# Performance work log

Hardware: AMD Instinct MI355X
Metric: run time of the kernel (lower is better)

The kernel has to match this reference:

```python
import jax, jax.numpy as jnp
import numpy as np

EPS = 2.220446049250313e-16  # sys.float_info.epsilon, matches CoCosNet feature_normalize

def feature_normalize(x):
    return x / (jnp.linalg.norm(x, axis=1, keepdims=True) + EPS)

def conv1x1(x, w, b):  # w: (out, in)
    return jnp.einsum('bchw,oc->bohw', x, w) + b[None, :, None, None]

def conv3x3(x, w, b):  # w: (out, in, 3, 3), SAME padding, stride 1
    y = jax.lax.conv_general_dilated(x, w, (1, 1), 'SAME',
                                     dimension_numbers=('NCHW', 'OIHW', 'NCHW'))
    return y + b[None, :, None, None]

@jax.custom_vjp
def sign_sig(x):
    return (x > 0).astype(x.dtype)

def _ss_fwd(x):
    return (x > 0).astype(x.dtype), jax.nn.sigmoid(x)

def _ss_bwd(s, g):
    return (g * s * (1.0 - s),)

sign_sig.defvjp(_ss_fwd, _ss_bwd)

def pono(x, eps=1e-5):  # PositionalNorm2d: normalize over channel dim
    m = jnp.mean(x, axis=1, keepdims=True)
    v = jnp.var(x, axis=1, keepdims=True)
    return (x - m) * jax.lax.rsqrt(v + eps)

def instance_norm(x, eps=1e-5):  # param-free, over spatial dims
    m = jnp.mean(x, axis=(2, 3), keepdims=True)
    v = jnp.var(x, axis=(2, 3), keepdims=True)
    return (x - m) * jax.lax.rsqrt(v + eps)

def setup_inputs() -> dict:
    B, CV, CPOS, H, W = 2, 256, 64, 64, 64
    CQK, DP, IC, NH = CV + CPOS, 64, 3, 128
    key = jax.random.key(0)
    ks = jax.random.split(key, 24)
    n = lambda i, s: jax.random.normal(ks[i], s, jnp.float32)
    w = lambda i, s: n(i, s) * 0.02
    z = lambda s: jnp.zeros(s, jnp.float32)
    return dict(
        q=n(0, (B, CV, H, W)), k=n(1, (B, CV, H, W)), v=n(2, (B, CV, H, W)),
        pos=n(3, (1, CPOS, H, W)),
        seg_map=jax.random.uniform(ks[4], (B, IC, H, W), jnp.float32),
        v2=n(5, (B, CV, H, W)),
        f_w=w(6, (CQK, CQK)), f_b=z(CQK),
        g_w=w(7, (CQK, CQK)), g_b=z(CQK),
        h_w=w(8, (CV, CV)), h_b=z(CV),
        fp_w=w(9, (DP, CQK)), fp_b=z(DP),
        gp_w=w(10, (DP, CQK)), gp_b=z(DP),
        sp_s_w=w(11, (NH, IC, 3, 3)), sp_s_b=z(NH),
        sp_g_w=w(12, (CV, NH, 3, 3)), sp_g_b=z(CV),
        sp_b_w=w(13, (CV, NH, 3, 3)), sp_b_b=z(CV),
        r1_w=w(14, (CV, CV, 3, 3)), r1_b=z(CV),
        r2_w=w(15, (CV, CV, 3, 3)), r2_b=z(CV),
    )

def reference(q, k, v, pos, seg_map, v2,
              f_w, f_b, g_w, g_b, h_w, h_b, fp_w, fp_b, gp_w, gp_b,
              sp_s_w, sp_s_b, sp_g_w, sp_g_b, sp_b_w, sp_b_b,
              r1_w, r1_b, r2_w, r2_b):
    b, cv, h, w = q.shape
    posb = jnp.broadcast_to(pos, (b,) + pos.shape[1:])
    query = jnp.concatenate([feature_normalize(q), posb], axis=1)
    keyt = jnp.concatenate([feature_normalize(k), posb], axis=1)
    qf = conv1x1(query, f_w, f_b)
    kf = conv1x1(keyt, g_w, g_b)
    vh = conv1x1(v, h_w, h_b)
    qp = conv1x1(query, fp_w, fp_b)
    kp = conv1x1(keyt, gp_w, gp_b)
    cqk = qf.shape[1]
    n = h * w
    Q = qf.reshape(b, cqk, n).transpose(0, 2, 1)          # (b, N, c_qk)
    K = kf.reshape(b, cqk, n)                             # (b, c_qk, N)
    V = vh.reshape(b, cv, n).transpose(0, 2, 1)           # (b, N, c_v)
    Qp = qp.reshape(b, -1, n).transpose(0, 2, 1)
    Kp = kp.reshape(b, -1, n)
    mask = sign_sig(jnp.einsum('bnc,bcm->bnm', Qp, Kp) / Kp.shape[1])
    cor = jnp.einsum('bnc,bcm->bnm', Q, K) / jnp.sqrt(jnp.float32(cqk))
    attn = jax.nn.softmax(cor, axis=-1)
    masked = attn * mask
    out = jnp.einsum('bnm,bmc->bnc', masked, V).transpose(0, 2, 1).reshape(b, cv, h, w)
    conf = masked.sum(-1).reshape(b, 1, h, w)
    V2 = v2.reshape(b, -1, n).transpose(0, 2, 1)
    attn2 = jax.nn.softmax(jnp.where(mask > 0, jnp.float32(-10000.0), cor), axis=-1)
    out2 = jnp.einsum('bnm,bmc->bnc', attn2, V2).transpose(0, 2, 1).reshape(b, -1, h, w)
    # SPADE(q, seg_map)
    actv = jax.nn.relu(conv3x3(seg_map, sp_s_w, sp_s_b))
    spade = instance_norm(q) * (1.0 + conv3x3(actv, sp_g_w, sp_g_b)) + conv3x3(actv, sp_b_w, sp_b_b)
    y = pono(out + (1.0 - conf) * spade + q)
    res = y + conv3x3(jax.nn.relu(conv3x3(y, r1_w, r1_b)), r2_w, r2_b)
    return (res, out2, cor)
```

## Files before the change

### kernel.cpp

```cpp
#include <hip/hip_runtime.h>
#include <stdint.h>


#define DEV static __device__ __forceinline__

typedef short short8 __attribute__((ext_vector_type(8)));
typedef float floatx4 __attribute__((ext_vector_type(4)));

DEV float bf2f(unsigned short b) { return __uint_as_float(((unsigned int)b) << 16); }
DEV unsigned short f2bf(float f) {
  unsigned int u = __float_as_uint(f);
  u += 0x7FFFu + ((u >> 16) & 1u);
  return (unsigned short)(u >> 16);
}
DEV float bfround(float f) { return bf2f(f2bf(f)); }

__global__ __launch_bounds__(256)
void cvt_f2b(const float* __restrict__ in, unsigned short* __restrict__ out, int n)
{
  int i = blockIdx.x * 256 + threadIdx.x;
  if (i < n) out[i] = f2bf(in[i]);
}

__global__ __launch_bounds__(256)
void prep_w9(const float* __restrict__ w, unsigned short* __restrict__ w9,
             int CO, int CI)
{
  int i = blockIdx.x * 256 + threadIdx.x;
  int tot = CO * CI * 9;
  if (i >= tot) return;
  int s = i % 9, rest = i / 9;
  int ci = rest % CI, o = rest / CI;
  w9[(long long)o * 9 * CI + s * CI + ci] = f2bf(w[i]);
}

__global__ __launch_bounds__(256)
void colnorm(const float* __restrict__ x, float* __restrict__ rnorm)
{
  int b = blockIdx.y, t = threadIdx.x;
  int n = (blockIdx.x << 5) + (t & 31);
  int cg = t >> 5;
  const float* base = x + ((long long)b << 20) + n;
  float s = 0.f;
#pragma unroll
  for (int c8 = 0; c8 < 32; c8++) {
    float v = base[((long long)(cg * 32 + c8)) << 12];
    s += v * v;
  }
  __shared__ float red[256];
  red[t] = s; __syncthreads();
  for (int st = 128; st >= 32; st >>= 1) {
    if (t < st) red[t] += red[t + st];
    __syncthreads();
  }
  if (t < 32)
    rnorm[(b << 12) + n] = 1.f / (sqrtf(red[t]) + 2.2204460492503131e-16f);
}

__global__ __launch_bounds__(256)
void build_qk3(const float* __restrict__ x, const float* __restrict__ pos,
               const float* __restrict__ rnorm, unsigned short* __restrict__ qt)
{
  __shared__ float tile[64][65];
  int b = blockIdx.z, by = blockIdx.y;
  int n0 = blockIdx.x << 6;
  int tx = threadIdx.x & 63, tg = threadIdx.x >> 6;
  const float* ib;
  int c0;
  if (by < 4) { ib = x + ((long long)b << 20) + ((long long)(by << 6) << 12); c0 = by << 6; }
  else        { ib = pos; c0 = 256; }
#pragma unroll
  for (int i = 0; i < 16; i++) {
    int r = tg * 16 + i;
    tile[r][tx] = ib[((long long)r << 12) + n0 + tx];
  }
  __syncthreads();
#pragma unroll
  for (int i = 0; i < 16; i++) {
    int r = tg * 16 + i;
    float sc = (by < 4) ? rnorm[(b << 12) + n0 + r] : 1.f;
    qt[((long long)(b * 4096 + n0 + r)) * 320 + c0 + tx] = f2bf(tile[tx][r] * sc);
  }
}

__global__ __launch_bounds__(256)
void transpose_c(const float* __restrict__ in, unsigned short* __restrict__ out, int C)
{
  __shared__ float tile[64][65];
  int b = blockIdx.z;
  int c0 = blockIdx.y << 6;
  int n0 = blockIdx.x << 6;
  const float* ib = in + (long long)b * C * 4096;
  unsigned short* ob = out + (long long)b * C * 4096;
  int tx = threadIdx.x & 63, tg = threadIdx.x >> 6;
#pragma unroll
  for (int i = 0; i < 16; i++) {
    int r = tg * 16 + i;
    tile[r][tx] = ib[((long long)(c0 + r) << 12) + n0 + tx];
  }
  __syncthreads();
#pragma unroll
  for (int i = 0; i < 16; i++) {
    int r = tg * 16 + i;
    ob[(long long)(n0 + r) * C + c0 + tx] = f2bf(tile[tx][r]);
  }
}

__global__ __launch_bounds__(256)
void gemm_bt(const unsigned short* __restrict__ A, long long sAb, int lda,
             const unsigned short* __restrict__ Bt, long long sBb, int ldb,
             int Ncols, int K, float alpha,
             const float* __restrict__ bias, int biasMode,
             unsigned short* __restrict__ Cb, long long sCbb, int ldcb,
             float* __restrict__ Cf, long long sCfb, int ldcf,
             unsigned short* __restrict__ Cm)
{
  __shared__ unsigned short As[128][40];
  __shared__ unsigned short Bs[128][40];
  int bz = blockIdx.z;
  const unsigned short* Ab = A + bz * sAb;
  const unsigned short* Bb = Bt + bz * sBb;
  int m0 = blockIdx.y << 7, n0 = blockIdx.x << 7;
  int t = threadIdx.x;
  int lane = t & 63, wave = t >> 6, quad = lane >> 4, l16 = lane & 15;
  int wm = (wave >> 1) << 6, wn = (wave & 1) << 6;

  floatx4 acc[4][4] = {};

  for (int k0 = 0; k0 < K; k0 += 32) {
#pragma unroll
    for (int s = 0; s < 2; s++) {
      int idx = t + (s << 8);
      int row = idx >> 2, ch = (idx & 3) << 3;
      short8 av = *(const short8*)(Ab + (long long)(m0 + row) * lda + k0 + ch);
      *(short8*)&As[row][ch] = av;
      short8 bv = {};
      if (n0 + row < Ncols) bv = *(const short8*)(Bb + (long long)(n0 + row) * ldb + k0 + ch);
      *(short8*)&Bs[row][ch] = bv;
    }
    __syncthreads();
    short8 af[4], bfv[4];
#pragma unroll
    for (int i = 0; i < 4; i++) af[i] = *(const short8*)&As[wm + (i << 4) + l16][quad << 3];
#pragma unroll
    for (int j = 0; j < 4; j++) bfv[j] = *(const short8*)&Bs[wn + (j << 4) + l16][quad << 3];
#pragma unroll
    for (int i = 0; i < 4; i++)
#pragma unroll
      for (int j = 0; j < 4; j++)
        acc[i][j] = __builtin_amdgcn_mfma_f32_16x16x32_bf16(af[i], bfv[j], acc[i][j], 0, 0, 0);
    __syncthreads();
  }

#pragma unroll
  for (int j = 0; j < 4; j++) {
    int col = n0 + wn + (j << 4) + l16;
    if (col >= Ncols) continue;
    float bcol = (biasMode == 1) ? bias[col] : 0.f;
#pragma unroll
    for (int i = 0; i < 4; i++) {
#pragma unroll
      for (int r = 0; r < 4; r++) {
        int row = m0 + wm + (i << 4) + (quad << 2) + r;
        float vv = acc[i][j][r] * alpha + bcol;
        if (biasMode == 2) vv += bias[row];
        if (Cb) Cb[bz * sCbb + (long long)row * ldcb + col] = f2bf(vv);
        if (Cf) Cf[bz * sCfb + (long long)row * ldcf + col] = bfround(vv);
        if (Cm) {
          unsigned long long bal = __ballot(vv > 0.f);
          if (l16 == 0)
            Cm[(long long)bz * 4096 * 256 + (long long)row * 256 + ((n0 + wn + (j << 4)) >> 4)]
              = (unsigned short)(bal >> (quad << 4));
        }
      }
    }
  }
}

__global__ __launch_bounds__(256)
void gemm_conv(const unsigned short* __restrict__ Xt, int CI,
               const unsigned short* __restrict__ W9, int CO,
               const float* __restrict__ bias,
               unsigned short* __restrict__ Cb, int relu,
               float* __restrict__ Cf, const float* __restrict__ addT, int rnd)
{
  __shared__ unsigned short As[128][40];
  __shared__ unsigned short Bs[128][40];
  int bz = blockIdx.z;
  const unsigned short* Xb = Xt + (long long)bz * 4096 * CI;
  int m0 = blockIdx.y << 7, n0 = blockIdx.x << 7;
  int t = threadIdx.x;
  int lane = t & 63, wave = t >> 6, quad = lane >> 4, l16 = lane & 15;
  int wm = (wave >> 1) << 6, wn = (wave & 1) << 6;
  int K9 = 9 * CI;

  floatx4 acc[4][4] = {};

  for (int tap = 0; tap < 9; ++tap) {
    int dy = tap / 3 - 1, dx = tap % 3 - 1;
    int off = dy * 64 + dx;
    for (int kc = 0; kc < CI; kc += 32) {
#pragma unroll
      for (int s = 0; s < 2; s++) {
        int idx = t + (s << 8);
        int row = idx >> 2, ch = (idx & 3) << 3;
        int p = m0 + row;
        int y = (p >> 6) + dy, x = (p & 63) + dx;
        short8 av = {};
        if ((unsigned)y < 64u && (unsigned)x < 64u)
          av = *(const short8*)(Xb + (long long)(p + off) * CI + kc + ch);
        *(short8*)&As[row][ch] = av;
        short8 bv = *(const short8*)(W9 + (long long)(n0 + row) * K9 + tap * CI + kc + ch);
        *(short8*)&Bs[row][ch] = bv;
      }
      __syncthreads();
      short8 af[4], bfv[4];
#pragma unroll
      for (int i = 0; i < 4; i++) af[i] = *(const short8*)&As[wm + (i << 4) + l16][quad << 3];
#pragma unroll
      for (int j = 0; j < 4; j++) bfv[j] = *(const short8*)&Bs[wn + (j << 4) + l16][quad << 3];
#pragma unroll
      for (int i = 0; i < 4; i++)
#pragma unroll
        for (int j = 0; j < 4; j++)
          acc[i][j] = __builtin_amdgcn_mfma_f32_16x16x32_bf16(af[i], bfv[j], acc[i][j], 0, 0, 0);
      __syncthreads();
    }
  }

#pragma unroll
  for (int j = 0; j < 4; j++) {
    int col = n0 + wn + (j << 4) + l16;
    float bcol = bias[col];
#pragma unroll
    for (int i = 0; i < 4; i++) {
#pragma unroll
      for (int r = 0; r < 4; r++) {
        int row = m0 + wm + (i << 4) + (quad << 2) + r;
        float vv = acc[i][j][r] + bcol;
        if (relu) vv = fmaxf(vv, 0.f);
        if (Cb) Cb[((long long)bz * 4096 + row) * CO + col] = f2bf(vv);
        if (Cf) {
          long long oi = ((long long)bz * CO + col) * 4096 + row;
          float ov = vv;
          if (addT) ov += addT[oi];
          Cf[oi] = rnd ? bfround(ov) : ov;
        }
      }
    }
  }
}

__global__ __launch_bounds__(256)
void stats_rows(const float* __restrict__ corF,
                const unsigned char* __restrict__ mbits,
                float4* __restrict__ statA, float* __restrict__ confF)
{
  long long row = blockIdx.x;
  const float4* cr = (const float4*)(corF + (row << 12));
  const unsigned char* mr = mbits + row * 512;
  int t = threadIdx.x;

  float lg[16]; unsigned int mk[16];
#pragma unroll
  for (int i = 0; i < 4; i++) {
    float4 cc = cr[i * 256 + t];
    unsigned char mb = mr[(i * 256 + t) >> 1];
    int sh = (t & 1) << 2;
    lg[4 * i + 0] = cc.x; lg[4 * i + 1] = cc.y;
    lg[4 * i + 2] = cc.z; lg[4 * i + 3] = cc.w;
#pragma unroll
    for (int j = 0; j < 4; j++) mk[4 * i + j] = (mb >> (sh + j)) & 1u;
  }
  float m1 = -3.0e38f, m2 = -3.0e38f; int cnt = 0;
#pragma unroll
  for (int e = 0; e < 16; e++) {
    m1 = fmaxf(m1, lg[e]);
    if (!mk[e]) m2 = fmaxf(m2, lg[e]);
    cnt += (int)mk[e];
  }
  __shared__ float4 red4[256];
  red4[t] = make_float4(m1, m2, 0.f, 0.f); __syncthreads();
  for (int s = 128; s > 0; s >>= 1) {
    if (t < s) {
      red4[t].x = fmaxf(red4[t].x, red4[t + s].x);
      red4[t].y = fmaxf(red4[t].y, red4[t + s].y);
    }
    __syncthreads();
  }
  float rmax1 = red4[0].x;
  float rmax2 = fmaxf(red4[0].y, -10000.f);
  __syncthreads();

  float s1 = 0.f, cn = 0.f, s2 = 0.f;
#pragma unroll
  for (int e = 0; e < 16; e++) {
    float ex = __expf(fminf(lg[e] - rmax1, 0.f));
    s1 += ex;
    if (mk[e]) cn += ex;
    else s2 += __expf(fminf(lg[e] - rmax2, 0.f));
  }
  red4[t] = make_float4(s1, cn, s2, (float)cnt); __syncthreads();
  for (int s = 128; s > 0; s >>= 1) {
    if (t < s) {
      red4[t].x += red4[t + s].x; red4[t].y += red4[t + s].y;
      red4[t].z += red4[t + s].z; red4[t].w += red4[t + s].w;
    }
    __syncthreads();
  }
  if (t == 0) {
    float4 r = red4[0];
    float sum2 = r.z + r.w * __expf(fminf(-10000.f - rmax2, 0.f));
    statA[row] = make_float4(rmax1, 1.f / fmaxf(r.x, 1e-30f),
                             rmax2, 1.f / fmaxf(sum2, 1e-30f));
    confF[row] = r.y / fmaxf(r.x, 1e-30f);
  }
}

__global__ __launch_bounds__(128, 3)
void gemm_pv3(const float* __restrict__ corF,
              const unsigned char* __restrict__ mbits,
              const float4* __restrict__ statA,
              const unsigned short* __restrict__ Bt0,
              const unsigned short* __restrict__ Bt1,
              float* __restrict__ Cf0, float* __restrict__ Cf1)
{
  __shared__ unsigned short As[32][40];
  __shared__ unsigned short Bs[128][40];
  int bz = blockIdx.z & 1, mode = blockIdx.z >> 1;
  const float* corb = corF + (long long)bz * 4096 * 4096;
  const unsigned char* mbb = mbits + (long long)bz * 4096 * 512;
  const unsigned short* Bb = (mode ? Bt1 : Bt0) + (long long)bz * 256 * 4096;
  int m0 = blockIdx.y << 5, n0 = blockIdx.x << 7;
  int t = threadIdx.x;
  int lane = t & 63, wave = t >> 6, quad = lane >> 4, l16 = lane & 15;
  int wn = wave << 6;

  int rA = t >> 2, cA = (t & 3) << 3;

  float4 sS = statA[(long long)bz * 4096 + m0 + rA];
  float rm, iv, mv;
  if (mode == 0) { rm = sS.x; iv = sS.y; mv = 0.f; }
  else { rm = sS.z; iv = sS.w; mv = __expf(fminf(-10000.f - rm, 0.f)) * iv; }

  floatx4 acc[2][4] = {};

  const float* cp_base = corb + (long long)(m0 + rA) * 4096 + cA;
  const unsigned char* mb_base = mbb + (long long)(m0 + rA) * 512 + (cA >> 3);
  const unsigned short* pb_base = Bb + (long long)(n0 + rA) * 4096 + cA;

  float4 pa0, pa1; short8 pb[4]; unsigned char pmb;
  auto issue = [&](int kk) {
    pa0 = *(const float4*)(cp_base + kk);
    pa1 = *(const float4*)(cp_base + kk + 4);
    pmb = mb_base[kk >> 3];
#pragma unroll
    for (int j = 0; j < 4; j++)
      pb[j] = *(const short8*)(pb_base + (long long)(j << 5) * 4096 + kk);
  };

  issue(0);
  for (int k0 = 0; k0 < 4096; k0 += 32) {
    {
      float cs[8] = {pa0.x, pa0.y, pa0.z, pa0.w, pa1.x, pa1.y, pa1.z, pa1.w};
      short8 av;
#pragma unroll
      for (int j = 0; j < 8; j++) {
        float p = __expf(cs[j] - rm) * iv;
        unsigned int mkb = (pmb >> j) & 1u;
        float val = mode ? (mkb ? mv : p) : (mkb ? p : 0.f);
        av[j] = (short)f2bf(val);
      }
      *(short8*)&As[rA][cA] = av;
#pragma unroll
      for (int j = 0; j < 4; j++)
        *(short8*)&Bs[rA + (j << 5)][cA] = pb[j];
    }
    __syncthreads();
    if (k0 + 32 < 4096) issue(k0 + 32);
    short8 af[2], bfv[4];
#pragma unroll
    for (int i = 0; i < 2; i++) af[i] = *(const short8*)&As[(i << 4) + l16][quad << 3];
#pragma unroll
    for (int j = 0; j < 4; j++) bfv[j] = *(const short8*)&Bs[wn + (j << 4) + l16][quad << 3];
#pragma unroll
    for (int i = 0; i < 2; i++)
#pragma unroll
      for (int j = 0; j < 4; j++)
        acc[i][j] = __builtin_amdgcn_mfma_f32_16x16x32_bf16(af[i], bfv[j], acc[i][j], 0, 0, 0);
    __syncthreads();
  }

#pragma unroll
  for (int j = 0; j < 4; j++) {
    int col = n0 + wn + (j << 4) + l16;
#pragma unroll
    for (int i = 0; i < 2; i++) {
#pragma unroll
      for (int r = 0; r < 4; r++) {
        int row = m0 + (i << 4) + (quad << 2) + r;
        float vv = bfround(acc[i][j][r]);
        if (mode) Cf1[(long long)bz * 256 * 4096 + (long long)col * 4096 + row] = vv;
        else      Cf0[(long long)bz * 4096 * 256 + (long long)row * 256 + col] = vv;
      }
    }
  }
}

__global__ __launch_bounds__(256)
void inorm_stats(const float* __restrict__ q, float* __restrict__ mu, float* __restrict__ rs)
{
  int c = blockIdx.x, b = blockIdx.y, t = threadIdx.x;
  const float* base = q + ((long long)(b * 256 + c) << 12);
  float s = 0.f, s2 = 0.f;
  for (int i = t; i < 4096; i += 256) { float v = base[i]; s += v; s2 += v * v; }
  __shared__ float r1[256], r2[256];
  r1[t] = s; r2[t] = s2; __syncthreads();
  for (int st = 128; st > 0; st >>= 1) {
    if (t < st) { r1[t] += r1[t + st]; r2[t] += r2[t + st]; }
    __syncthreads();
  }
  if (t == 0) {
    float m = r1[0] * (1.f / 4096.f);
    float var = fmaxf(r2[0] * (1.f / 4096.f) - m * m, 0.f);
    mu[b * 256 + c] = m;
    rs[b * 256 + c] = rsqrtf(var + 1e-5f);
  }
}

__global__ __launch_bounds__(256)
void conv3x3(const float* __restrict__ inF,
             const float* __restrict__ wgt, const float* __restrict__ bias,
             int CI, int CO, const float* __restrict__ addF,
             float* __restrict__ outF, int relu, int rnd)
{
  __shared__ float wsm[2304];
  int b = blockIdx.z, o = blockIdx.y, t = threadIdx.x;
  for (int i = t; i < CI * 9; i += 256) wsm[i] = wgt[(long long)o * CI * 9 + i];
  __syncthreads();
  int x = t & 63, y = (blockIdx.x << 2) + (t >> 6);
  bool ym = y > 0, yp = y < 63, xm = x > 0, xp = x < 63;
  int p = y * 64 + x;
  long long ibase = ((long long)b * CI) << 12;
  float acc = bias[o];
  for (int ci = 0; ci < CI; ci++) {
    const float* wp = &wsm[ci * 9];
    long long ib = ibase + ((long long)ci << 12) + p;
    float v00 = (ym && xm) ? inF[ib - 65] : 0.f;
    float v01 = ym ? inF[ib - 64] : 0.f;
    float v02 = (ym && xp) ? inF[ib - 63] : 0.f;
    float v10 = xm ? inF[ib - 1] : 0.f;
    float v11 = inF[ib];
    float v12 = xp ? inF[ib + 1] : 0.f;
    float v20 = (yp && xm) ? inF[ib + 63] : 0.f;
    float v21 = yp ? inF[ib + 64] : 0.f;
    float v22 = (yp && xp) ? inF[ib + 65] : 0.f;
    acc += v00 * wp[0] + v01 * wp[1] + v02 * wp[2]
         + v10 * wp[3] + v11 * wp[4] + v12 * wp[5]
         + v20 * wp[6] + v21 * wp[7] + v22 * wp[8];
  }
  if (relu) acc = fmaxf(acc, 0.f);
  long long oidx = (((long long)(b * CO + o)) << 12) + p;
  if (addF) acc += addF[oidx];
  outF[oidx] = rnd ? bfround(acc) : acc;
}

__global__ __launch_bounds__(256)
void pono_y(const float* __restrict__ outF, const float* __restrict__ confF,
            const float* __restrict__ gF, const float* __restrict__ bF,
            const float* __restrict__ q, const float* __restrict__ mu,
            const float* __restrict__ rs, float* __restrict__ yF,
            unsigned short* __restrict__ yT)
{
  int n = blockIdx.x, b = blockIdx.y, c = threadIdx.x;
  long long cn = ((long long)(b * 256 + c) << 12) + n;
  float qv = q[cn];
  float sp = (qv - mu[b * 256 + c]) * rs[b * 256 + c] * (1.f + gF[cn]) + bF[cn];
  float cf = confF[b * 4096 + n];
  float tv = outF[((long long)(b * 4096 + n) << 8) + c] + (1.f - cf) * sp + qv;
  __shared__ float red[256];
  red[c] = tv; __syncthreads();
  for (int s = 128; s > 0; s >>= 1) { if (c < s) red[c] += red[c + s]; __syncthreads(); }
  float m = red[0] * (1.f / 256.f); __syncthreads();
  float d = tv - m;
  red[c] = d * d; __syncthreads();
  for (int s = 128; s > 0; s >>= 1) { if (c < s) red[c] += red[c + s]; __syncthreads(); }
  float var = fmaxf(red[0] * (1.f / 256.f), 0.f);
  float yv = d * rsqrtf(var + 1e-5f);
  yF[cn] = yv;
  yT[((long long)(b * 4096 + n) << 8) + c] = f2bf(yv);
}


extern "C" void kernel_launch(void* const* d_in, const int* in_sizes, int n_in,
                              void* d_out, int out_size, void* d_ws, size_t ws_size,
                              hipStream_t stream)
{
  (void)in_sizes; (void)n_in; (void)out_size; (void)ws_size;
  const int B = 2, CV = 256, CQK = 320, DP = 64, N = 4096, NH = 128, IC = 3;
  const float INV_SQRT_CQK = 0.05590169943749474241f;

  const float* q    = (const float*)d_in[0];
  const float* k    = (const float*)d_in[1];
  const float* v    = (const float*)d_in[2];
  const float* pos  = (const float*)d_in[3];
  const float* seg  = (const float*)d_in[4];
  const float* v2   = (const float*)d_in[5];
  const float* f_w  = (const float*)d_in[6];
  const float* f_b  = (const float*)d_in[7];
  const float* g_w  = (const float*)d_in[8];
  const float* g_b  = (const float*)d_in[9];
  const float* h_w  = (const float*)d_in[10];
  const float* h_b  = (const float*)d_in[11];
  const float* fp_w = (const float*)d_in[12];
  const float* fp_b = (const float*)d_in[13];
  const float* gp_w = (const float*)d_in[14];
  const float* gp_b = (const float*)d_in[15];
  const float* sp_s_w = (const float*)d_in[16];
  const float* sp_s_b = (const float*)d_in[17];
  const float* sp_g_w = (const float*)d_in[18];
  const float* sp_g_b = (const float*)d_in[19];
  const float* sp_b_w = (const float*)d_in[20];
  const float* sp_b_b = (const float*)d_in[21];
  const float* r1_w = (const float*)d_in[22];
  const float* r1_b = (const float*)d_in[23];
  const float* r2_w = (const float*)d_in[24];
  const float* r2_b = (const float*)d_in[25];

  float* res_o  = (float*)d_out;
  float* out2_o = res_o + (long long)B * CV * N;
  float* cor_o  = res_o + 2ll * B * CV * N;

  unsigned short* query_t = (unsigned short*)cor_o;
  unsigned short* keyt_t  = query_t + (long long)B * N * CQK;
  float*          outBuf  = res_o;

  char* wp_ = (char*)d_ws;
  auto take = [&](size_t bytes) -> void* {
    void* r = wp_; wp_ += (bytes + 255) & ~(size_t)255; return r;
  };
  unsigned short* v_t     = (unsigned short*)take((size_t)B * N * CV * 2);
  unsigned short* qf_t    = (unsigned short*)take((size_t)B * N * CQK * 2);
  unsigned short* kf_t    = (unsigned short*)take((size_t)B * N * CQK * 2);
  unsigned short* qp_t    = (unsigned short*)take((size_t)B * N * DP * 2);
  unsigned short* kp_t    = (unsigned short*)take((size_t)B * N * DP * 2);
  unsigned short* vh      = (unsigned short*)take((size_t)B * CV * N * 2);
  unsigned short* v2b     = (unsigned short*)take((size_t)B * CV * N * 2);
  unsigned short* fwB     = (unsigned short*)take((size_t)CQK * CQK * 2);
  unsigned short* gwB     = (unsigned short*)take((size_t)CQK * CQK * 2);
  unsigned short* fpwB    = (unsigned short*)take((size_t)DP * CQK * 2);
  unsigned short* gpwB    = (unsigned short*)take((size_t)DP * CQK * 2);
  unsigned short* hwB     = (unsigned short*)take((size_t)CV * CV * 2);
  unsigned short* maskB16 = (unsigned short*)take((size_t)B * N * 256 * 2);
  float4*         statA   = (float4*)take((size_t)B * N * 16);
  float*          confF   = (float*)take((size_t)B * N * 4);
  float*          muF     = (float*)take((size_t)B * CV * 4);
  float*          rsF     = (float*)take((size_t)B * CV * 4);
  float*          rnormQ  = (float*)take((size_t)B * N * 4);
  float*          rnormK  = (float*)take((size_t)B * N * 4);
  float*          actv    = (float*)take((size_t)B * NH * N * 4);
  float*          gC      = (float*)take((size_t)B * CV * N * 4);
  float*          bC      = (float*)take((size_t)B * CV * N * 4);
  float*          yF      = (float*)take((size_t)B * CV * N * 4);
  unsigned short* spgW9   = (unsigned short*)take((size_t)CV * 9 * NH * 2);
  unsigned short* spbW9   = (unsigned short*)take((size_t)CV * 9 * NH * 2);
  unsigned short* r1W9    = (unsigned short*)take((size_t)CV * 9 * CV * 2);
  unsigned short* r2W9    = (unsigned short*)take((size_t)CV * 9 * CV * 2);
  unsigned short* yT      = qf_t;
  unsigned short* a1T     = kf_t;
  unsigned short* actvT   = v_t;

  dim3 blk(256);
  auto cvt = [&](const float* in, unsigned short* out, int n) {
    cvt_f2b<<<dim3((n + 255) / 256), blk, 0, stream>>>(in, out, n);
  };
  auto prepw = [&](const float* w, unsigned short* w9, int CO, int CI) {
    prep_w9<<<dim3((CO * CI * 9 + 255) / 256), blk, 0, stream>>>(w, w9, CO, CI);
  };
  auto gemm = [&](const unsigned short* A, long long sAb, int lda,
                  const unsigned short* Bt, long long sBb, int ldb,
                  int M, int Nc, int K, float alpha,
                  const float* bias, int biasMode,
                  unsigned short* Cb, long long sCbb, int ldcb,
                  float* Cf, long long sCfb, int ldcf,
                  unsigned short* Cm) {
    dim3 grid((Nc + 127) / 128, M / 128, B);
    gemm_bt<<<grid, blk, 0, stream>>>(A, sAb, lda, Bt, sBb, ldb, Nc, K, alpha,
                                      bias, biasMode, Cb, sCbb, ldcb,
                                      Cf, sCfb, ldcf, Cm);
  };
  auto conv = [&](const unsigned short* Xt, int CI, const unsigned short* W9,
                  const float* bias, unsigned short* Cb, int relu,
                  float* Cf, const float* addT, int rnd) {
    gemm_conv<<<dim3(CV / 128, N / 128, B), blk, 0, stream>>>(
        Xt, CI, W9, CV, bias, Cb, relu, Cf, addT, rnd);
  };

  cvt(f_w, fwB, CQK * CQK);
  cvt(g_w, gwB, CQK * CQK);
  cvt(fp_w, fpwB, DP * CQK);
  cvt(gp_w, gpwB, DP * CQK);
  cvt(h_w, hwB, CV * CV);
  cvt(v2, v2b, B * CV * N);
  prepw(sp_g_w, spgW9, CV, NH);
  prepw(sp_b_w, spbW9, CV, NH);
  prepw(r1_w, r1W9, CV, CV);
  prepw(r2_w, r2W9, CV, CV);

  colnorm<<<dim3(128, B), blk, 0, stream>>>(q, rnormQ);
  colnorm<<<dim3(128, B), blk, 0, stream>>>(k, rnormK);
  build_qk3<<<dim3(64, 5, B), blk, 0, stream>>>(q, pos, rnormQ, query_t);
  build_qk3<<<dim3(64, 5, B), blk, 0, stream>>>(k, pos, rnormK, keyt_t);
  transpose_c<<<dim3(64, 4, B), blk, 0, stream>>>(v, v_t, CV);

  gemm(query_t, (long long)N * CQK, CQK, fwB, 0, CQK, N, CQK, CQK, 1.f, f_b, 1,
       qf_t, (long long)N * CQK, CQK, nullptr, 0, 0, nullptr);
  gemm(keyt_t, (long long)N * CQK, CQK, gwB, 0, CQK, N, CQK, CQK, 1.f, g_b, 1,
       kf_t, (long long)N * CQK, CQK, nullptr, 0, 0, nullptr);
  gemm(query_t, (long long)N * CQK, CQK, fpwB, 0, CQK, N, DP, CQK, 1.f, fp_b, 1,
       qp_t, (long long)N * DP, DP, nullptr, 0, 0, nullptr);
  gemm(keyt_t, (long long)N * CQK, CQK, gpwB, 0, CQK, N, DP, CQK, 1.f, gp_b, 1,
       kp_t, (long long)N * DP, DP, nullptr, 0, 0, nullptr);
  gemm(hwB, 0, CV, v_t, (long long)N * CV, CV, CV, N, CV, 1.f, h_b, 2,
       vh, (long long)CV * N, N, nullptr, 0, 0, nullptr);

  gemm(qf_t, (long long)N * CQK, CQK, kf_t, (long long)N * CQK, CQK, N, N, CQK,
       INV_SQRT_CQK, nullptr, 0, nullptr, 0, 0,
       cor_o, (long long)N * N, N, nullptr);
  gemm(qp_t, (long long)N * DP, DP, kp_t, (long long)N * DP, DP, N, N, DP, 1.f,
       nullptr, 0, nullptr, 0, 0, nullptr, 0, 0, maskB16);

  stats_rows<<<dim3(B * N), blk, 0, stream>>>(cor_o, (const unsigned char*)maskB16,
                                              statA, confF);
  gemm_pv3<<<dim3(2, 128, 2 * B), dim3(128), 0, stream>>>(
      cor_o, (const unsigned char*)maskB16, statA, vh, v2b, outBuf, out2_o);

  inorm_stats<<<dim3(CV, B), blk, 0, stream>>>(q, muF, rsF);
  conv3x3<<<dim3(16, NH, B), blk, 0, stream>>>(seg, sp_s_w, sp_s_b, IC, NH, nullptr, actv, 1, 0);
  transpose_c<<<dim3(64, 2, B), blk, 0, stream>>>(actv, actvT, NH);
  conv(actvT, NH, spgW9, sp_g_b, nullptr, 0, gC, nullptr, 0);
  conv(actvT, NH, spbW9, sp_b_b, nullptr, 0, bC, nullptr, 0);
  pono_y<<<dim3(N, B), blk, 0, stream>>>(outBuf, confF, gC, bC, q, muF, rsF, yF, yT);
  conv(yT, CV, r1W9, r1_b, a1T, 1, nullptr, nullptr, 0);
  conv(a1T, CV, r2W9, r2_b, nullptr, 0, res_o, yF, 1);
}
```

Before: 838.7 us.

## Widen PV GEMM tile to full 256 columns and defer softmax normalization

The fused softmax-times-V kernel now uses 256-thread blocks that cover all 256 output columns per 32-row tile. Each exp(cor) tile is therefore computed once, where before it was recomputed for each of two column halves. The 1/sum normalization moves from the per-element exp to the epilogue, and the exponent uses exp2f with a prescaled log2e. Conversion to bf16 uses the packed v_cvt_pk_bf16_f32 instruction. The block count halves and the LDS B tile doubles, which may lower occupancy. Applying the normalization after accumulation in bf16 slightly changes rounding.

```diff
diff --git a/kernel.cpp b/kernel.cpp
--- a/kernel.cpp
+++ b/kernel.cpp
@@ -317,8 +317,8 @@
   }
 }
 
-__global__ __launch_bounds__(128, 3)
-void gemm_pv3(const float* __restrict__ corF,
+__global__ __launch_bounds__(256, 2)
+void gemm_pv4(const float* __restrict__ corF,
               const unsigned char* __restrict__ mbits,
               const float4* __restrict__ statA,
               const unsigned short* __restrict__ Bt0,
@@ -326,55 +326,64 @@
               float* __restrict__ Cf0, float* __restrict__ Cf1)
 {
   __shared__ unsigned short As[32][40];
-  __shared__ unsigned short Bs[128][40];
-  int bz = blockIdx.z & 1, mode = blockIdx.z >> 1;
+  __shared__ unsigned short Bs[256][40];
+  __shared__ float2 sstat[32];
+  int bz = blockIdx.y & 1, mode = blockIdx.y >> 1;
   const float* corb = corF + (long long)bz * 4096 * 4096;
   const unsigned char* mbb = mbits + (long long)bz * 4096 * 512;
   const unsigned short* Bb = (mode ? Bt1 : Bt0) + (long long)bz * 256 * 4096;
-  int m0 = blockIdx.y << 5, n0 = blockIdx.x << 7;
+  int m0 = blockIdx.x << 5;
   int t = threadIdx.x;
   int lane = t & 63, wave = t >> 6, quad = lane >> 4, l16 = lane & 15;
   int wn = wave << 6;
-
-  int rA = t >> 2, cA = (t & 3) << 3;
-
-  float4 sS = statA[(long long)bz * 4096 + m0 + rA];
-  float rm, iv, mv;
-  if (mode == 0) { rm = sS.x; iv = sS.y; mv = 0.f; }
-  else { rm = sS.z; iv = sS.w; mv = __expf(fminf(-10000.f - rm, 0.f)) * iv; }
+  const float L2E = 1.44269504088896340736f;
+
+  if (t < 32) {
+    float4 s = statA[(long long)bz * 4096 + m0 + t];
+    float rm = mode ? s.z : s.x, iv = mode ? s.w : s.y;
+    sstat[t] = make_float2(-rm * L2E, iv);
+  }
+  __syncthreads();
+
+  int rA = t >> 3, cA = (t & 7) << 2;
+  int rB = t >> 2, cB = (t & 3) << 3;
+  float nrmL = sstat[rA].x;
+  float mvr = exp2f(-10000.f * L2E + nrmL);
 
   floatx4 acc[2][4] = {};
 
-  const float* cp_base = corb + (long long)(m0 + rA) * 4096 + cA;
-  const unsigned char* mb_base = mbb + (long long)(m0 + rA) * 512 + (cA >> 3);
-  const unsigned short* pb_base = Bb + (long long)(n0 + rA) * 4096 + cA;
-
-  float4 pa0, pa1; short8 pb[4]; unsigned char pmb;
+  const float* cpb = corb + (long long)(m0 + rA) * 4096 + cA;
+  const unsigned char* mbp = mbb + (long long)(m0 + rA) * 512;
+  const unsigned short* pbb = Bb + (long long)rB * 4096 + cB;
+
+  float4 pa; short8 pb[4]; unsigned int pmk;
   auto issue = [&](int kk) {
-    pa0 = *(const float4*)(cp_base + kk);
-    pa1 = *(const float4*)(cp_base + kk + 4);
-    pmb = mb_base[kk >> 3];
+    pa = *(const float4*)(cpb + kk);
+    pmk = (unsigned int)(mbp[(kk + cA) >> 3] >> (cA & 7)) & 0xFu;
 #pragma unroll
     for (int j = 0; j < 4; j++)
-      pb[j] = *(const short8*)(pb_base + (long long)(j << 5) * 4096 + kk);
+      pb[j] = *(const short8*)(pbb + (long long)(j << 6) * 4096 + kk);
   };
 
   issue(0);
   for (int k0 = 0; k0 < 4096; k0 += 32) {
     {
-      float cs[8] = {pa0.x, pa0.y, pa0.z, pa0.w, pa1.x, pa1.y, pa1.z, pa1.w};
-      short8 av;
-#pragma unroll
-      for (int j = 0; j < 8; j++) {
-        float p = __expf(cs[j] - rm) * iv;
-        unsigned int mkb = (pmb >> j) & 1u;
-        float val = mode ? (mkb ? mv : p) : (mkb ? p : 0.f);
-        av[j] = (short)f2bf(val);
+      float cs[4] = {pa.x, pa.y, pa.z, pa.w};
+      float vs[4];
+#pragma unroll
+      for (int j = 0; j < 4; j++) {
+        float e = exp2f(fmaf(cs[j], L2E, nrmL));
+        bool mk = (pmk >> j) & 1u;
+        vs[j] = mode ? (mk ? mvr : e) : (mk ? e : 0.f);
       }
-      *(short8*)&As[rA][cA] = av;
+      unsigned int u01, u23;
+      asm("v_cvt_pk_bf16_f32 %0, %1, %2" : "=v"(u01) : "v"(vs[0]), "v"(vs[1]));
+      asm("v_cvt_pk_bf16_f32 %0, %1, %2" : "=v"(u23) : "v"(vs[2]), "v"(vs[3]));
+      *(unsigned int*)&As[rA][cA] = u01;
+      *(unsigned int*)&As[rA][cA + 2] = u23;
 #pragma unroll
       for (int j = 0; j < 4; j++)
-        *(short8*)&Bs[rA + (j << 5)][cA] = pb[j];
+        *(short8*)&Bs[rB + (j << 6)][cB] = pb[j];
     }
     __syncthreads();
     if (k0 + 32 < 4096) issue(k0 + 32);
@@ -393,13 +402,14 @@
 
 #pragma unroll
   for (int j = 0; j < 4; j++) {
-    int col = n0 + wn + (j << 4) + l16;
+    int col = wn + (j << 4) + l16;
 #pragma unroll
     for (int i = 0; i < 2; i++) {
 #pragma unroll
       for (int r = 0; r < 4; r++) {
-        int row = m0 + (i << 4) + (quad << 2) + r;
-        float vv = bfround(acc[i][j][r]);
+        int lrow = (i << 4) + (quad << 2) + r;
+        int row = m0 + lrow;
+        float vv = bfround(acc[i][j][r] * sstat[lrow].y);
         if (mode) Cf1[(long long)bz * 256 * 4096 + (long long)col * 4096 + row] = vv;
         else      Cf0[(long long)bz * 4096 * 256 + (long long)row * 256 + col] = vv;
       }
@@ -632,7 +642,7 @@
 
   stats_rows<<<dim3(B * N), blk, 0, stream>>>(cor_o, (const unsigned char*)maskB16,
                                               statA, confF);
-  gemm_pv3<<<dim3(2, 128, 2 * B), dim3(128), 0, stream>>>(
+  gemm_pv4<<<dim3(128, 2 * B), blk, 0, stream>>>(
       cor_o, (const unsigned char*)maskB16, statA, vh, v2b, outBuf, out2_o);
 
   inorm_stats<<<dim3(CV, B), blk, 0, stream>>>(q, muF, rsF);
```

Result: no change. 825.3 us (-1.6%).
